# Kernel optimization log

Measured on AMD Instinct MI355X. Metric: run time of the kernel, lower is better.

The kernel has to match this reference:

```python
import jax, jax.numpy as jnp
import numpy as np

B, S, D, H, DH = 2, 2048, 1024, 16, 64
LN_EPS = 1e-5

def _layernorm(x, g, b):
    mu = jnp.mean(x, axis=-1, keepdims=True)
    var = jnp.mean(jnp.square(x - mu), axis=-1, keepdims=True)
    return (x - mu) * jax.lax.rsqrt(var + LN_EPS) * g + b

def setup_inputs() -> dict:
    key = jax.random.key(0)
    ks = jax.random.split(key, 12)
    s = 0.02
    return {
        'x': jax.random.normal(ks[0], (B, S, D), jnp.float32),
        'attention_mask': jnp.zeros((B, S), jnp.bool_),
        'Wq': jax.random.normal(ks[1], (H, D, DH), jnp.float32) * s,
        'bq': jnp.zeros((H, DH), jnp.float32),
        'Wk': jax.random.normal(ks[2], (H, D, DH), jnp.float32) * s,
        'bk': jnp.zeros((H, DH), jnp.float32),
        'Wv': jax.random.normal(ks[3], (H, D, DH), jnp.float32) * s,
        'bv': jnp.zeros((H, DH), jnp.float32),
        'ln_g': jnp.ones((D,), jnp.float32),
        'ln_b': jnp.zeros((D,), jnp.float32),
        'W1': jax.random.normal(ks[4], (D, 4 * D), jnp.float32) * s,
        'b1': jnp.zeros((4 * D,), jnp.float32),
        'W2': jax.random.normal(ks[5], (4 * D, D), jnp.float32) * s,
        'b2': jnp.zeros((D,), jnp.float32),
    }

def reference(x, attention_mask, Wq, bq, Wk, bk, Wv, bv, ln_g, ln_b, W1, b1, W2, b2):
    # NOTE: source has a typo bug ('attentoin_score'), so the attention_mask is
    # computed-then-discarded; softmax is applied to the UNMASKED scaled scores.
    dh = Wq.shape[-1]
    q = jnp.einsum('bsd,hde->bhse', x, Wq) + bq[:, None, :]  # [B,H,S,dh]
    k = jnp.einsum('bsd,hde->bhse', x, Wk) + bk[:, None, :]
    v = jnp.einsum('bsd,hde->bhse', x, Wv) + bv[:, None, :]
    scores = jnp.einsum('bhse,bhte->bhst', q, k) / jnp.sqrt(jnp.float32(dh))
    attn = jax.nn.softmax(scores, axis=-1)
    o = jnp.einsum('bhst,bhte->bhse', attn, v)  # [B,H,S,dh]
    b_, h_, s_, e_ = o.shape
    # concat heads along last dim == transpose then reshape
    mha = jnp.transpose(o, (0, 2, 1, 3)).reshape(b_, s_, h_ * e_)
    h1 = _layernorm(x + mha, ln_g, ln_b)
    ffn = jax.nn.relu(h1 @ W1 + b1) @ W2 + b2
    return _layernorm(h1 + ffn, ln_g, ln_b)
```

## Files before the change

### kernel.cpp

```cpp
#include <hip/hip_runtime.h>

#define DEVI __device__ __forceinline__

typedef __attribute__((ext_vector_type(8))) __bf16 bf16x8;
typedef __attribute__((ext_vector_type(4))) float f32x4;
typedef __attribute__((ext_vector_type(4))) unsigned short u16x4;
typedef __attribute__((ext_vector_type(8))) unsigned short u16x8;

static DEVI unsigned short f2bf(float f) {
  unsigned int i = __float_as_uint(f);
  i += 0x7fffu + ((i >> 16) & 1u);
  return (unsigned short)(i >> 16);
}

static DEVI unsigned short f2bfh(float f) {
  union { __bf16 h; unsigned short u; } c;
  c.h = (__bf16)f;
  return c.u;
}

static DEVI f32x4 mfma16x16x32(bf16x8 a, bf16x8 b, f32x4 c) {
  return __builtin_amdgcn_mfma_f32_16x16x32_bf16(a, b, c, 0, 0, 0);
}

static DEVI void async_ld16(const void* g, void* lds) {
  __builtin_amdgcn_global_load_lds(
      (const __attribute__((address_space(1))) void*)g,
      (__attribute__((address_space(3))) void*)lds, 16, 0, 0);
}

template <int BN, int OUT_MODE, bool RELU>
static DEVI void gemm_bt_core(const unsigned short* __restrict__ A, int lda,
                              const unsigned short* __restrict__ Bt, int ldb,
                              int K, int m0, int n0,
                              const float* __restrict__ bias,
                              void* __restrict__ Cp, int ldc,
                              const float* __restrict__ bq,
                              const float* __restrict__ bk,
                              const float* __restrict__ bv,
                              unsigned short* __restrict__ qo,
                              unsigned short* __restrict__ ko,
                              unsigned short* __restrict__ vo) {
  constexpr int MT = (BN == 128) ? 4 : 2;
  constexpr int NT = 4;
  __shared__ __align__(16) unsigned short As[128 * 32];
  __shared__ __align__(16) unsigned short Bs[BN * 32];

  const int tid = threadIdx.x;
  const int w = tid >> 6, l = tid & 63;
  const int lr = l & 15, lq = l >> 4;
  const int wm0 = (BN == 128) ? ((w >> 1) * 64) : (w * 32);
  const int wn0 = (BN == 128) ? ((w & 1) * 64) : 0;
  const int lrow = l >> 2;
  const int lcol = (l & 3) * 8;

  f32x4 acc[MT][NT];
#pragma unroll
  for (int i = 0; i < MT; ++i)
#pragma unroll
    for (int j = 0; j < NT; ++j) acc[i][j] = (f32x4){0.f, 0.f, 0.f, 0.f};

  for (int kb = 0; kb < K; kb += 32) {
#pragma unroll
    for (int p = 0; p < 2; ++p) {
      const int r0 = p * 64 + w * 16;
      async_ld16(A + (size_t)(m0 + r0 + lrow) * lda + kb + lcol, As + r0 * 32);
    }
#pragma unroll
    for (int p = 0; p < BN / 64; ++p) {
      const int r0 = p * 64 + w * 16;
      async_ld16(Bt + (size_t)(n0 + r0 + lrow) * ldb + kb + lcol, Bs + r0 * 32);
    }
    __syncthreads();

    bf16x8 af[MT], bfr[NT];
#pragma unroll
    for (int mt = 0; mt < MT; ++mt)
      af[mt] = *(const bf16x8*)(As + (wm0 + mt * 16 + lr) * 32 + lq * 8);
#pragma unroll
    for (int nt = 0; nt < NT; ++nt)
      bfr[nt] = *(const bf16x8*)(Bs + (wn0 + nt * 16 + lr) * 32 + lq * 8);
#pragma unroll
    for (int mt = 0; mt < MT; ++mt)
#pragma unroll
      for (int nt = 0; nt < NT; ++nt)
        acc[mt][nt] = mfma16x16x32(af[mt], bfr[nt], acc[mt][nt]);
    __syncthreads();
  }

#pragma unroll
  for (int mt = 0; mt < MT; ++mt) {
    const int grow = m0 + wm0 + mt * 16 + lq * 4;
#pragma unroll
    for (int nt = 0; nt < NT; ++nt) {
      const int gcol = n0 + wn0 + nt * 16 + lr;
      if (OUT_MODE == 2) {
        const int which = gcol >> 10;
        const int h = (gcol >> 6) & 15;
        const int e = gcol & 63;
        const float* bp = (which == 0) ? bq : (which == 1) ? bk : bv;
        const float bvv = bp[gcol & 1023];
        unsigned short* op = (which == 0) ? qo : (which == 1) ? ko : vo;
#pragma unroll
        for (int r = 0; r < 4; ++r) {
          const int row = grow + r;
          const int b_ = row >> 11, s_ = row & 2047;
          const size_t base = (size_t)((b_ << 4) + h) * 131072 + (size_t)s_ * 64;
          if (which == 1) {
            const int o = e >> 3;
            const int pos = (((o ^ (s_ & 7)) << 3) | (e & 7));
            op[base + pos] = f2bf((acc[mt][nt][r] + bvv) * 0.18033688011112f);
          } else {
            op[base + e] = f2bf(acc[mt][nt][r] + bvv);
          }
        }
      } else if (OUT_MODE == 3) {
#pragma unroll
        for (int r = 0; r < 4; ++r)
          ((unsigned short*)Cp)[(size_t)(grow + r) * ldc + gcol] =
              f2bf(acc[mt][nt][r]);
      } else {
        const float bvv = bias[gcol];
#pragma unroll
        for (int r = 0; r < 4; ++r) {
          float val = acc[mt][nt][r] + bvv;
          if (RELU) val = fmaxf(val, 0.f);
          if (OUT_MODE == 1)
            ((unsigned short*)Cp)[(size_t)(grow + r) * ldc + gcol] = f2bf(val);
          else
            ((float*)Cp)[(size_t)(grow + r) * ldc + gcol] = val;
        }
      }
    }
  }
}

__global__ __launch_bounds__(256) void k_gemm_qkv(
    const unsigned short* __restrict__ xb, const unsigned short* __restrict__ Wt,
    const float* __restrict__ bq, const float* __restrict__ bk,
    const float* __restrict__ bv, unsigned short* __restrict__ qo,
    unsigned short* __restrict__ ko, unsigned short* __restrict__ vo) {
  gemm_bt_core<128, 2, false>(xb, 1024, Wt, 1024, 1024, blockIdx.x * 128,
                              blockIdx.y * 128, nullptr, nullptr, 0, bq, bk, bv,
                              qo, ko, vo);
}

__global__ __launch_bounds__(256) void k_ffn1(
    const unsigned short* __restrict__ h1b, const unsigned short* __restrict__ W1t,
    const float* __restrict__ b1, unsigned short* __restrict__ f1) {
  gemm_bt_core<128, 1, true>(h1b, 1024, W1t, 1024, 1024, blockIdx.x * 128,
                             blockIdx.y * 128, b1, f1, 4096, nullptr, nullptr,
                             nullptr, nullptr, nullptr, nullptr);
}

__global__ __launch_bounds__(256) void k_ffn2(
    const unsigned short* __restrict__ f1, const unsigned short* __restrict__ W2t,
    unsigned short* __restrict__ p0, unsigned short* __restrict__ p1) {
  const int z = blockIdx.z;
  unsigned short* p = z ? p1 : p0;
  gemm_bt_core<64, 3, false>(f1 + z * 2048, 4096, W2t + z * 2048, 4096, 2048,
                             blockIdx.x * 128, blockIdx.y * 64, nullptr, p, 1024,
                             nullptr, nullptr, nullptr, nullptr, nullptr,
                             nullptr);
}

__global__ __launch_bounds__(256) void k_cvt(const float* __restrict__ src,
                                             unsigned short* __restrict__ dst) {
  const size_t i = ((size_t)blockIdx.x * 256 + threadIdx.x) * 4;
  f32x4 v = *(const f32x4*)(src + i);
  u16x4 pk;
#pragma unroll
  for (int j = 0; j < 4; ++j) pk[j] = f2bf(v[j]);
  *(u16x4*)(dst + i) = pk;
}

static DEVI void tr64(const float* __restrict__ s, int sld,
                      unsigned short* __restrict__ d, int dld) {
  __shared__ float t[64][65];
  const int tr = threadIdx.x >> 4;
  const int tc4 = (threadIdx.x & 15) * 4;
#pragma unroll
  for (int i = 0; i < 4; ++i) {
    f32x4 v = *(const f32x4*)(s + (size_t)(i * 16 + tr) * sld + tc4);
#pragma unroll
    for (int j = 0; j < 4; ++j) t[i * 16 + tr][tc4 + j] = v[j];
  }
  __syncthreads();
#pragma unroll
  for (int i = 0; i < 4; ++i) {
    const int c = i * 16 + tr;
    u16x4 pk;
#pragma unroll
    for (int j = 0; j < 4; ++j) pk[j] = f2bf(t[tc4 + j][c]);
    *(u16x4*)(d + (size_t)c * dld + tc4) = pk;
  }
}

__global__ __launch_bounds__(256) void k_tw(const float* __restrict__ src,
                                            unsigned short* __restrict__ dst,
                                            int C) {
  const int R = (int)gridDim.x * 64;
  const int r0 = blockIdx.x * 64, c0 = blockIdx.y * 64;
  tr64(src + (size_t)r0 * C + c0, C, dst + (size_t)c0 * R + r0, R);
}

__global__ __launch_bounds__(256) void k_twqkv(const float* __restrict__ Wq,
                                               const float* __restrict__ Wk,
                                               const float* __restrict__ Wv,
                                               unsigned short* __restrict__ dst) {
  const int which = blockIdx.y >> 4, h = blockIdx.y & 15;
  const float* W = (which == 0) ? Wq : (which == 1) ? Wk : Wv;
  const float* s = W + (size_t)h * 65536;
  unsigned short* d = dst + (size_t)(which * 1024 + h * 64) * 1024;
  const int r0 = blockIdx.x * 64;
  tr64(s + (size_t)r0 * 64, 64, d + r0, 1024);
}

__global__ __launch_bounds__(256) void k_vprep(const unsigned short* __restrict__ vb,
                                               unsigned short* __restrict__ vp) {
  const int bh = blockIdx.y, t = blockIdx.x;
  __shared__ unsigned short tl[64][72];
  const int tid = threadIdx.x;
  const size_t base = (size_t)bh * 131072;
  const int kr = tid >> 3, oc = tid & 7;
#pragma unroll
  for (int p = 0; p < 2; ++p) {
    const int key = p * 32 + kr;
    *(u16x8*)&tl[key][oc * 8] =
        *(const u16x8*)(vb + base + (size_t)(t * 64 + key) * 64 + oc * 8);
  }
  __syncthreads();
#pragma unroll
  for (int p = 0; p < 2; ++p) {
    const int dh = p * 32 + kr;
    const int ok = oc ^ (dh & 7);
    u16x8 pk;
#pragma unroll
    for (int j = 0; j < 8; ++j) {
      const int kap = ok * 8 + j;
      const int key = (kap & 3) * 16 + (kap >> 2);
      pk[j] = tl[key][dh];
    }
    *(u16x8*)(vp + base + (size_t)dh * 2048 + t * 64 + oc * 8) = pk;
  }
}

__global__ __launch_bounds__(512) void k_attn(
    const unsigned short* __restrict__ q, const unsigned short* __restrict__ ks,
    const unsigned short* __restrict__ vp, float* __restrict__ mha) {
  const int bid = blockIdx.x;
  const int bh = (bid & 7) * 4 + ((bid >> 3) >> 4);
  const int qt = (bid >> 3) & 15;
  const int b = bh >> 4, h = bh & 15;
  const int tid = threadIdx.x;
  const int w = tid >> 6, l = tid & 63;
  const int lr = l & 15, lq = l >> 4, l7 = lr & 7;

  __shared__ __align__(16) unsigned short Ks[2][64 * 64];
  __shared__ __align__(16) unsigned short Vt[2][64 * 64];
  __shared__ __align__(16) unsigned short Ps[8][16][72];

  const size_t bho = (size_t)bh * 131072;
  const int q0 = qt * 128 + w * 16;

  bf16x8 qf0, qf1;
  {
    const unsigned short* qp = q + bho + (size_t)(q0 + lr) * 64 + lq * 8;
    qf0 = *(const bf16x8*)qp;
    qf1 = *(const bf16x8*)(qp + 32);
  }

  f32x4 l_acc[4];
  f32x4 o[4];
#pragma unroll
  for (int i = 0; i < 4; ++i) {
    l_acc[i] = (f32x4){0.f, 0.f, 0.f, 0.f};
    o[i] = (f32x4){0.f, 0.f, 0.f, 0.f};
  }

  const unsigned short* kg = ks + bho;
  const unsigned short* vg = vp + bho;
  const int srow = l >> 3, scol = (l & 7) * 8;
  const int r0 = w * 8;

  async_ld16(kg + (size_t)(r0 + srow) * 64 + scol, &Ks[0][r0 * 64]);
  async_ld16(vg + (size_t)(r0 + srow) * 2048 + scol, &Vt[0][r0 * 64]);
  __syncthreads();

  for (int kt = 0; kt < 32; ++kt) {
    const int cur = kt & 1, nxt = cur ^ 1;
    if (kt + 1 < 32) {
      const int k1 = (kt + 1) * 64;
      async_ld16(kg + (size_t)(k1 + r0 + srow) * 64 + scol, &Ks[nxt][r0 * 64]);
      async_ld16(vg + (size_t)(r0 + srow) * 2048 + k1 + scol, &Vt[nxt][r0 * 64]);
    }

    bf16x8 kf[4][2];
#pragma unroll
    for (int ct = 0; ct < 4; ++ct)
#pragma unroll
      for (int hh = 0; hh < 2; ++hh)
        kf[ct][hh] = *(const bf16x8*)&Ks[cur][(ct * 16 + lr) * 64 +
                                             (((hh << 2) | lq) ^ l7) * 8];
    f32x4 s[4];
#pragma unroll
    for (int ct = 0; ct < 4; ++ct) {
      f32x4 t = {0.f, 0.f, 0.f, 0.f};
      t = mfma16x16x32(qf0, kf[ct][0], t);
      t = mfma16x16x32(qf1, kf[ct][1], t);
      s[ct] = t;
    }

#pragma unroll
    for (int r = 0; r < 4; ++r) {
      f32x4 pe;
#pragma unroll
      for (int ct = 0; ct < 4; ++ct)
        pe[ct] = __builtin_amdgcn_exp2f(s[ct][r]);
      l_acc[r] += pe;
      u16x4 pk;
#pragma unroll
      for (int ct = 0; ct < 4; ++ct) pk[ct] = f2bfh(pe[ct]);
      *(u16x4*)&Ps[w][lq * 4 + r][lr * 4] = pk;
    }
    __asm__ volatile("" ::: "memory");

    bf16x8 vf[4][2];
#pragma unroll
    for (int dt = 0; dt < 4; ++dt)
#pragma unroll
      for (int hh = 0; hh < 2; ++hh)
        vf[dt][hh] = *(const bf16x8*)&Vt[cur][(dt * 16 + lr) * 64 +
                                             (((hh << 2) | lq) ^ l7) * 8];
    bf16x8 pf0 = *(const bf16x8*)&Ps[w][lr][lq * 8];
    bf16x8 pf1 = *(const bf16x8*)&Ps[w][lr][32 + lq * 8];
#pragma unroll
    for (int dt = 0; dt < 4; ++dt) {
      o[dt] = mfma16x16x32(pf0, vf[dt][0], o[dt]);
      o[dt] = mfma16x16x32(pf1, vf[dt][1], o[dt]);
    }
    __syncthreads();
  }

#pragma unroll
  for (int r = 0; r < 4; ++r) {
    f32x4 la = l_acc[r];
    float sd = la[0] + la[1] + la[2] + la[3];
    sd += __shfl_xor(sd, 1);
    sd += __shfl_xor(sd, 2);
    sd += __shfl_xor(sd, 4);
    sd += __shfl_xor(sd, 8);
    const float inv = 1.f / sd;
    float* op = mha + ((size_t)b * 2048 + q0 + lq * 4 + r) * 1024 + h * 64 + lr;
    op[0] = o[0][r] * inv;
    op[16] = o[1][r] * inv;
    op[32] = o[2][r] * inv;
    op[48] = o[3][r] * inv;
  }
}

__global__ __launch_bounds__(256) void k_add_ln(const float* __restrict__ a,
                                                const float* __restrict__ b,
                                                const float* __restrict__ g,
                                                const float* __restrict__ be,
                                                float* __restrict__ out,
                                                unsigned short* __restrict__ outb) {
  const int row = blockIdx.x;
  const int tid = threadIdx.x;
  const size_t base = (size_t)row * 1024 + tid * 4;
  f32x4 va = *(const f32x4*)(a + base);
  f32x4 vb = *(const f32x4*)(b + base);
  f32x4 xx;
  float s = 0.f, q = 0.f;
#pragma unroll
  for (int i = 0; i < 4; ++i) {
    xx[i] = va[i] + vb[i];
    s += xx[i];
    q += xx[i] * xx[i];
  }
#pragma unroll
  for (int off = 1; off < 64; off <<= 1) {
    s += __shfl_xor(s, off);
    q += __shfl_xor(q, off);
  }
  __shared__ float ss[4], qs[4];
  const int w = tid >> 6;
  if ((tid & 63) == 0) { ss[w] = s; qs[w] = q; }
  __syncthreads();
  s = ss[0] + ss[1] + ss[2] + ss[3];
  q = qs[0] + qs[1] + qs[2] + qs[3];
  const float mean = s * (1.f / 1024.f);
  const float var = q * (1.f / 1024.f) - mean * mean;
  const float rstd = rsqrtf(var + 1e-5f);
  f32x4 vg = *(const f32x4*)(g + tid * 4);
  f32x4 vbe = *(const f32x4*)(be + tid * 4);
  f32x4 ov;
#pragma unroll
  for (int i = 0; i < 4; ++i) ov[i] = (xx[i] - mean) * rstd * vg[i] + vbe[i];
  *(f32x4*)(out + base) = ov;
  if (outb) {
    u16x4 pk;
#pragma unroll
    for (int i = 0; i < 4; ++i) pk[i] = f2bf(ov[i]);
    *(u16x4*)(outb + base) = pk;
  }
}

__global__ __launch_bounds__(256) void k_add_ln3(
    const float* __restrict__ a, const unsigned short* __restrict__ p0,
    const unsigned short* __restrict__ p1, const float* __restrict__ cb,
    const float* __restrict__ g, const float* __restrict__ be,
    float* __restrict__ out) {
  const int row = blockIdx.x;
  const int tid = threadIdx.x;
  const size_t base = (size_t)row * 1024 + tid * 4;
  f32x4 va = *(const f32x4*)(a + base);
  u16x4 u0 = *(const u16x4*)(p0 + base);
  u16x4 u1 = *(const u16x4*)(p1 + base);
  f32x4 vcb = *(const f32x4*)(cb + tid * 4);
  f32x4 xx;
  float s = 0.f, q = 0.f;
#pragma unroll
  for (int i = 0; i < 4; ++i) {
    const float f0 = __uint_as_float((unsigned int)u0[i] << 16);
    const float f1 = __uint_as_float((unsigned int)u1[i] << 16);
    xx[i] = va[i] + f0 + f1 + vcb[i];
    s += xx[i];
    q += xx[i] * xx[i];
  }
#pragma unroll
  for (int off = 1; off < 64; off <<= 1) {
    s += __shfl_xor(s, off);
    q += __shfl_xor(q, off);
  }
  __shared__ float ss[4], qs[4];
  const int w = tid >> 6;
  if ((tid & 63) == 0) { ss[w] = s; qs[w] = q; }
  __syncthreads();
  s = ss[0] + ss[1] + ss[2] + ss[3];
  q = qs[0] + qs[1] + qs[2] + qs[3];
  const float mean = s * (1.f / 1024.f);
  const float var = q * (1.f / 1024.f) - mean * mean;
  const float rstd = rsqrtf(var + 1e-5f);
  f32x4 vg = *(const f32x4*)(g + tid * 4);
  f32x4 vbe = *(const f32x4*)(be + tid * 4);
  f32x4 ov;
#pragma unroll
  for (int i = 0; i < 4; ++i) ov[i] = (xx[i] - mean) * rstd * vg[i] + vbe[i];
  *(f32x4*)(out + base) = ov;
}

extern "C" void kernel_launch(void* const* d_in, const int* in_sizes, int n_in,
                              void* d_out, int out_size, void* d_ws,
                              size_t ws_size, hipStream_t stream) {
  const float* x = (const float*)d_in[0];
  const float* Wq = (const float*)d_in[2];
  const float* bq = (const float*)d_in[3];
  const float* Wk = (const float*)d_in[4];
  const float* bk = (const float*)d_in[5];
  const float* Wv = (const float*)d_in[6];
  const float* bv = (const float*)d_in[7];
  const float* lg = (const float*)d_in[8];
  const float* lb = (const float*)d_in[9];
  const float* W1 = (const float*)d_in[10];
  const float* b1 = (const float*)d_in[11];
  const float* W2 = (const float*)d_in[12];
  const float* b2 = (const float*)d_in[13];

  char* ws = (char*)d_ws;
  const size_t MB = 1024 * 1024;
  unsigned short* qb = (unsigned short*)(ws + 0);
  unsigned short* kb = (unsigned short*)(ws + 8 * MB);
  unsigned short* vb = (unsigned short*)(ws + 16 * MB);
  unsigned short* vp = (unsigned short*)(ws + 24 * MB);
  unsigned short* w2t = (unsigned short*)(ws + 0);
  unsigned short* f1 = (unsigned short*)(ws + 8 * MB);
  unsigned short* xb = (unsigned short*)(ws + 40 * MB);
  float* mha = (float*)(ws + 40 * MB);
  unsigned short* p1 = (unsigned short*)(ws + 40 * MB);
  float* h1 = (float*)(ws + 56 * MB);
  unsigned short* h1b = (unsigned short*)(ws + 72 * MB);
  unsigned short* p0 = (unsigned short*)(ws + 72 * MB);
  unsigned short* wqkvt = (unsigned short*)(ws + 80 * MB);
  unsigned short* w1t = (unsigned short*)(ws + 86 * MB);

  k_cvt<<<dim3(4096), 256, 0, stream>>>(x, xb);
  k_twqkv<<<dim3(16, 48), 256, 0, stream>>>(Wq, Wk, Wv, wqkvt);
  k_tw<<<dim3(16, 64), 256, 0, stream>>>(W1, w1t, 4096);

  k_gemm_qkv<<<dim3(32, 24), 256, 0, stream>>>(xb, wqkvt, bq, bk, bv, qb, kb, vb);
  k_vprep<<<dim3(32, 32), 256, 0, stream>>>(vb, vp);
  k_attn<<<dim3(512), 512, 0, stream>>>(qb, kb, vp, mha);

  k_tw<<<dim3(64, 16), 256, 0, stream>>>(W2, w2t, 1024);
  k_add_ln<<<dim3(4096), 256, 0, stream>>>(x, mha, lg, lb, h1, h1b);
  k_ffn1<<<dim3(32, 32), 256, 0, stream>>>(h1b, w1t, b1, f1);
  k_ffn2<<<dim3(32, 16, 2), 256, 0, stream>>>(f1, w2t, p0, p1);
  k_add_ln3<<<dim3(4096), 256, 0, stream>>>(h1, p0, p1, b2, lg, lb,
                                            (float*)d_out);
}
```

Baseline: 329.1 us.

## Merge weight transposes, drop fp32 h1, use 4-way split-K FFN2 with 128-wide tiles

Folds the three weight-transpose launches (QKV, W1, W2) into one kernel. The first layernorm now writes only a bf16 h1, which the final layernorm reads back as its residual instead of an fp32 copy. FFN2 becomes a 4-way split-K GEMM with 128x128 tiles, producing four bf16 partials that the final layernorm sums. The goal is fewer launches and less memory traffic. In exchange the partial-sum traffic grows and the residual loses precision to bf16.

```diff
diff --git a/kernel.cpp b/kernel.cpp
--- a/kernel.cpp
+++ b/kernel.cpp
@@ -17,6 +17,10 @@
   union { __bf16 h; unsigned short u; } c;
   c.h = (__bf16)f;
   return c.u;
+}
+
+static DEVI float bf2f(unsigned short u) {
+  return __uint_as_float((unsigned int)u << 16);
 }
 
 static DEVI f32x4 mfma16x16x32(bf16x8 a, bf16x8 b, f32x4 c) {
@@ -155,13 +159,13 @@
 
 __global__ __launch_bounds__(256) void k_ffn2(
     const unsigned short* __restrict__ f1, const unsigned short* __restrict__ W2t,
-    unsigned short* __restrict__ p0, unsigned short* __restrict__ p1) {
+    unsigned short* __restrict__ pbase) {
   const int z = blockIdx.z;
-  unsigned short* p = z ? p1 : p0;
-  gemm_bt_core<64, 3, false>(f1 + z * 2048, 4096, W2t + z * 2048, 4096, 2048,
-                             blockIdx.x * 128, blockIdx.y * 64, nullptr, p, 1024,
-                             nullptr, nullptr, nullptr, nullptr, nullptr,
-                             nullptr);
+  unsigned short* p = pbase + (size_t)z * 4194304;
+  gemm_bt_core<128, 3, false>(f1 + z * 1024, 4096, W2t + z * 1024, 4096, 1024,
+                              blockIdx.x * 128, blockIdx.y * 128, nullptr, p,
+                              1024, nullptr, nullptr, nullptr, nullptr, nullptr,
+                              nullptr);
 }
 
 __global__ __launch_bounds__(256) void k_cvt(const float* __restrict__ src,
@@ -196,24 +200,31 @@
   }
 }
 
-__global__ __launch_bounds__(256) void k_tw(const float* __restrict__ src,
-                                            unsigned short* __restrict__ dst,
-                                            int C) {
-  const int R = (int)gridDim.x * 64;
-  const int r0 = blockIdx.x * 64, c0 = blockIdx.y * 64;
-  tr64(src + (size_t)r0 * C + c0, C, dst + (size_t)c0 * R + r0, R);
-}
-
-__global__ __launch_bounds__(256) void k_twqkv(const float* __restrict__ Wq,
-                                               const float* __restrict__ Wk,
-                                               const float* __restrict__ Wv,
-                                               unsigned short* __restrict__ dst) {
-  const int which = blockIdx.y >> 4, h = blockIdx.y & 15;
-  const float* W = (which == 0) ? Wq : (which == 1) ? Wk : Wv;
-  const float* s = W + (size_t)h * 65536;
-  unsigned short* d = dst + (size_t)(which * 1024 + h * 64) * 1024;
-  const int r0 = blockIdx.x * 64;
-  tr64(s + (size_t)r0 * 64, 64, d + r0, 1024);
+__global__ __launch_bounds__(256) void k_twall(
+    const float* __restrict__ Wq, const float* __restrict__ Wk,
+    const float* __restrict__ Wv, const float* __restrict__ W1,
+    const float* __restrict__ W2, unsigned short* __restrict__ wqkvt,
+    unsigned short* __restrict__ w1t, unsigned short* __restrict__ w2t) {
+  const int bid = blockIdx.x;
+  if (bid < 768) {
+    const int bx = bid & 15, by = bid >> 4;
+    const int which = by >> 4, h = by & 15;
+    const float* W = (which == 0) ? Wq : (which == 1) ? Wk : Wv;
+    const float* s = W + (size_t)h * 65536;
+    unsigned short* d = wqkvt + (size_t)(which * 1024 + h * 64) * 1024;
+    const int r0 = bx * 64;
+    tr64(s + (size_t)r0 * 64, 64, d + r0, 1024);
+  } else if (bid < 1792) {
+    const int t = bid - 768;
+    const int bx = t & 15, by = t >> 4;
+    const int r0 = bx * 64, c0 = by * 64;
+    tr64(W1 + (size_t)r0 * 4096 + c0, 4096, w1t + (size_t)c0 * 1024 + r0, 1024);
+  } else {
+    const int t = bid - 1792;
+    const int bx = t & 63, by = t >> 6;
+    const int r0 = bx * 64, c0 = by * 64;
+    tr64(W2 + (size_t)r0 * 1024 + c0, 1024, w2t + (size_t)c0 * 4096 + r0, 4096);
+  }
 }
 
 __global__ __launch_bounds__(256) void k_vprep(const unsigned short* __restrict__ vb,
@@ -363,7 +374,6 @@
                                                 const float* __restrict__ b,
                                                 const float* __restrict__ g,
                                                 const float* __restrict__ be,
-                                                float* __restrict__ out,
                                                 unsigned short* __restrict__ outb) {
   const int row = blockIdx.x;
   const int tid = threadIdx.x;
@@ -394,39 +404,36 @@
   const float rstd = rsqrtf(var + 1e-5f);
   f32x4 vg = *(const f32x4*)(g + tid * 4);
   f32x4 vbe = *(const f32x4*)(be + tid * 4);
-  f32x4 ov;
-#pragma unroll
-  for (int i = 0; i < 4; ++i) ov[i] = (xx[i] - mean) * rstd * vg[i] + vbe[i];
-  *(f32x4*)(out + base) = ov;
-  if (outb) {
-    u16x4 pk;
-#pragma unroll
-    for (int i = 0; i < 4; ++i) pk[i] = f2bf(ov[i]);
-    *(u16x4*)(outb + base) = pk;
-  }
-}
-
-__global__ __launch_bounds__(256) void k_add_ln3(
-    const float* __restrict__ a, const unsigned short* __restrict__ p0,
-    const unsigned short* __restrict__ p1, const float* __restrict__ cb,
-    const float* __restrict__ g, const float* __restrict__ be,
-    float* __restrict__ out) {
+  u16x4 pk;
+#pragma unroll
+  for (int i = 0; i < 4; ++i)
+    pk[i] = f2bf((xx[i] - mean) * rstd * vg[i] + vbe[i]);
+  *(u16x4*)(outb + base) = pk;
+}
+
+__global__ __launch_bounds__(256) void k_add_ln4(
+    const unsigned short* __restrict__ h1b, const unsigned short* __restrict__ pb,
+    const float* __restrict__ cb, const float* __restrict__ g,
+    const float* __restrict__ be, float* __restrict__ out) {
   const int row = blockIdx.x;
   const int tid = threadIdx.x;
   const size_t base = (size_t)row * 1024 + tid * 4;
-  f32x4 va = *(const f32x4*)(a + base);
-  u16x4 u0 = *(const u16x4*)(p0 + base);
-  u16x4 u1 = *(const u16x4*)(p1 + base);
+  u16x4 uh = *(const u16x4*)(h1b + base);
+  u16x4 up[4];
+#pragma unroll
+  for (int z = 0; z < 4; ++z)
+    up[z] = *(const u16x4*)(pb + base + (size_t)z * 4194304);
   f32x4 vcb = *(const f32x4*)(cb + tid * 4);
   f32x4 xx;
   float s = 0.f, q = 0.f;
 #pragma unroll
   for (int i = 0; i < 4; ++i) {
-    const float f0 = __uint_as_float((unsigned int)u0[i] << 16);
-    const float f1 = __uint_as_float((unsigned int)u1[i] << 16);
-    xx[i] = va[i] + f0 + f1 + vcb[i];
-    s += xx[i];
-    q += xx[i] * xx[i];
+    float v = bf2f(uh[i]) + vcb[i];
+#pragma unroll
+    for (int z = 0; z < 4; ++z) v += bf2f(up[z][i]);
+    xx[i] = v;
+    s += v;
+    q += v * v;
   }
 #pragma unroll
   for (int off = 1; off < 64; off <<= 1) {
@@ -473,29 +480,23 @@
   unsigned short* kb = (unsigned short*)(ws + 8 * MB);
   unsigned short* vb = (unsigned short*)(ws + 16 * MB);
   unsigned short* vp = (unsigned short*)(ws + 24 * MB);
-  unsigned short* w2t = (unsigned short*)(ws + 0);
-  unsigned short* f1 = (unsigned short*)(ws + 8 * MB);
-  unsigned short* xb = (unsigned short*)(ws + 40 * MB);
+  unsigned short* f1 = (unsigned short*)(ws + 0);
+  unsigned short* xb = (unsigned short*)(ws + 32 * MB);
+  unsigned short* pb = (unsigned short*)(ws + 32 * MB);
   float* mha = (float*)(ws + 40 * MB);
-  unsigned short* p1 = (unsigned short*)(ws + 40 * MB);
-  float* h1 = (float*)(ws + 56 * MB);
-  unsigned short* h1b = (unsigned short*)(ws + 72 * MB);
-  unsigned short* p0 = (unsigned short*)(ws + 72 * MB);
-  unsigned short* wqkvt = (unsigned short*)(ws + 80 * MB);
-  unsigned short* w1t = (unsigned short*)(ws + 86 * MB);
+  unsigned short* h1b = (unsigned short*)(ws + 64 * MB);
+  unsigned short* wqkvt = (unsigned short*)(ws + 72 * MB);
+  unsigned short* w1t = (unsigned short*)(ws + 78 * MB);
+  unsigned short* w2t = (unsigned short*)(ws + 86 * MB);
 
   k_cvt<<<dim3(4096), 256, 0, stream>>>(x, xb);
-  k_twqkv<<<dim3(16, 48), 256, 0, stream>>>(Wq, Wk, Wv, wqkvt);
-  k_tw<<<dim3(16, 64), 256, 0, stream>>>(W1, w1t, 4096);
+  k_twall<<<dim3(2816), 256, 0, stream>>>(Wq, Wk, Wv, W1, W2, wqkvt, w1t, w2t);
 
   k_gemm_qkv<<<dim3(32, 24), 256, 0, stream>>>(xb, wqkvt, bq, bk, bv, qb, kb, vb);
   k_vprep<<<dim3(32, 32), 256, 0, stream>>>(vb, vp);
   k_attn<<<dim3(512), 512, 0, stream>>>(qb, kb, vp, mha);
-
-  k_tw<<<dim3(64, 16), 256, 0, stream>>>(W2, w2t, 1024);
-  k_add_ln<<<dim3(4096), 256, 0, stream>>>(x, mha, lg, lb, h1, h1b);
+  k_add_ln<<<dim3(4096), 256, 0, stream>>>(x, mha, lg, lb, h1b);
   k_ffn1<<<dim3(32, 32), 256, 0, stream>>>(h1b, w1t, b1, f1);
-  k_ffn2<<<dim3(32, 16, 2), 256, 0, stream>>>(f1, w2t, p0, p1);
-  k_add_ln3<<<dim3(4096), 256, 0, stream>>>(h1, p0, p1, b2, lg, lb,
-                                            (float*)d_out);
-}
+  k_ffn2<<<dim3(32, 8, 4), 256, 0, stream>>>(f1, w2t, pb);
+  k_add_ln4<<<dim3(4096), 256, 0, stream>>>(h1b, pb, b2, lg, lb, (float*)d_out);
+}
```

Result: no change. 324.0 us (-1.5%).
